# Optimization experiments

Hardware: AMD Instinct MI355X
Metric: run time of the kernel (lower is better)

The kernel has to match this reference:

```python
import jax, jax.numpy as jnp
import numpy as np

N_NODES = 100000
D = 128


def setup_inputs() -> dict:
    key = jax.random.key(0)
    ks = jax.random.split(key, 6)
    x = jax.random.normal(ks[0], (N_NODES, 300), dtype=jnp.float32)
    n_id = jnp.arange(N_NODES, dtype=jnp.int64)
    edge_index = jax.random.randint(ks[1], (2, 1600000), 0, N_NODES, dtype=jnp.int64)
    history = jax.random.randint(ks[2], (4096, 50), 0, N_NODES, dtype=jnp.int64)
    candidates = jax.random.randint(ks[3], (4096, 20), 0, N_NODES, dtype=jnp.int64)
    W_enc = jax.random.normal(ks[4], (300, D), dtype=jnp.float32) * 0.05
    W_gnn = jax.random.normal(ks[5], (D, D), dtype=jnp.float32) * 0.05
    return {"x": x, "n_id": n_id, "edge_index": edge_index,
            "history": history, "candidates": candidates,
            "W_enc": W_enc, "W_gnn": W_gnn}


def reference(x, n_id, edge_index, history, candidates, W_enc, W_gnn):
    N = x.shape[0]
    # news encoder: linear projection of raw node features -> [N, D]
    news_emb = x @ W_enc
    # gnn: mean aggregation over incoming edges, then linear
    src, dst = edge_index[0], edge_index[1]
    agg = jax.ops.segment_sum(news_emb[src], dst, num_segments=N)      # [N, D]
    deg = jax.ops.segment_sum(jnp.ones((src.shape[0], 1), news_emb.dtype), dst,
                              num_segments=N)                          # [N, 1]
    struct_emb = (agg / jnp.maximum(deg, 1.0)) @ W_gnn
    xx = news_emb + struct_emb                                          # [N, D]
    # scatter into dense lookup table (n_id == arange -> max_id == N, static)
    news_lookup = jnp.zeros((N, xx.shape[1]), xx.dtype).at[n_id].set(xx)
    # gather histories / candidates
    history_embs = news_lookup[history]                                 # [B, H, D]
    cand_embs = news_lookup[candidates]                                 # [B, C, D]
    mask = (history != 0).astype(xx.dtype)                              # [B, H]
    sum_embs = jnp.einsum('bhd,bh->bd', history_embs, mask)
    num_read = jnp.clip(mask.sum(axis=1, keepdims=True), 1e-9, None)
    user_vec = sum_embs / num_read                                      # [B, D]
    scores = jnp.einsum('bcd,bd->bc', cand_embs, user_vec)              # [B, C]
    return scores
```

## Files before the change

kernel.cpp:

```cpp
#include <hip/hip_runtime.h>

#define NN 100000
#define DD 128
#define KE 300
#define NE 1600000
#define NB 4096
#define HL 50
#define CL 20

#define NBUCK 1563
#define SLOT  1280
#define PBLK  250
#define EPB   6400
#define EPT   25
#define EBLK  1563

#define WTE_N 40960
#define WTG_N 16384

typedef unsigned short ushort_t;
using bf16x8 = __attribute__((ext_vector_type(8))) short;
using f32x4  = __attribute__((ext_vector_type(4))) float;

union U4B { uint4 u; bf16x8 b; unsigned a[4]; };

__device__ __forceinline__ ushort_t f2bf(float f) {
    unsigned u = __float_as_uint(f);
    unsigned r = u + 0x7FFF + ((u >> 16) & 1);
    return (ushort_t)(r >> 16);
}
__device__ __forceinline__ float bf2f(unsigned s) {
    return __uint_as_float(s << 16);
}
__device__ __forceinline__ bf16x8 pack8(float4 a, float4 b) {
    U4B r;
    r.a[0] = (unsigned)f2bf(a.x) | ((unsigned)f2bf(a.y) << 16);
    r.a[1] = (unsigned)f2bf(a.z) | ((unsigned)f2bf(a.w) << 16);
    r.a[2] = (unsigned)f2bf(b.x) | ((unsigned)f2bf(b.y) << 16);
    r.a[3] = (unsigned)f2bf(b.z) | ((unsigned)f2bf(b.w) << 16);
    return r.b;
}

__global__ __launch_bounds__(256) void prep_w(const float* __restrict__ We,
                                              const float* __restrict__ Wg,
                                              ushort_t* __restrict__ wte,
                                              ushort_t* __restrict__ wtg) {
    int i = blockIdx.x * 256 + threadIdx.x;
    if (i < WTE_N) {
        int j = i & 7, lane = (i >> 3) & 63, cf = (i >> 9) & 7, ch = i >> 12;
        int k = ch * 32 + (lane >> 4) * 8 + j;
        int n = cf * 16 + (lane & 15);
        wte[i] = f2bf((k < KE) ? We[k * DD + n] : 0.f);
    } else if (i < WTE_N + WTG_N) {
        int t = i - WTE_N;
        int j = t & 7, lane = (t >> 3) & 63, cf = (t >> 9) & 7, ks = t >> 12;
        int k = ks * 32 + (lane >> 4) * 8 + j;
        int n = cf * 16 + (lane & 15);
        wtg[t] = f2bf(Wg[k * DD + n]);
    }
}

__device__ __forceinline__ bf16x8 loadA8(const float* __restrict__ x,
                                         int row, int col, bool rowok) {
    float v[8];
    if (rowok && col + 8 <= KE) {
        const float4* p = (const float4*)&x[(long long)row * KE + col];
        float4 a = p[0], b = p[1];
        v[0]=a.x; v[1]=a.y; v[2]=a.z; v[3]=a.w;
        v[4]=b.x; v[5]=b.y; v[6]=b.z; v[7]=b.w;
    } else {
#pragma unroll
        for (int j = 0; j < 8; ++j) {
            int c = col + j;
            v[j] = (rowok && c < KE) ? x[(long long)row * KE + c] : 0.f;
        }
    }
    return pack8(make_float4(v[0], v[1], v[2], v[3]),
                 make_float4(v[4], v[5], v[6], v[7]));
}

__global__ __launch_bounds__(256) void k_front(const float* __restrict__ x,
                                               const ushort_t* __restrict__ wtF,
                                               const int* __restrict__ ei,
                                               unsigned* __restrict__ gcur,
                                               unsigned* __restrict__ pairs,
                                               ushort_t* __restrict__ news) {
    __shared__ unsigned sh[NBUCK], sb[NBUCK], sc[NBUCK];
    const int tid = threadIdx.x;

    if (blockIdx.x < PBLK) {
        const int eb = blockIdx.x * EPB;
        for (int i = tid; i < NBUCK; i += 256) sh[i] = 0;
        __syncthreads();

        unsigned val[EPT], bk[EPT];
#pragma unroll
        for (int l = 0; l < EPT; ++l) {
            int e = eb + l * 256 + tid;
            unsigned src = (unsigned)ei[e];
            unsigned dst = (unsigned)ei[NE + e];
            val[l] = (src << 6) | (dst & 63u);
            bk[l] = dst >> 6;
            atomicAdd(&sh[bk[l]], 1u);
        }
        __syncthreads();

        for (int i = tid; i < NBUCK; i += 256) {
            unsigned h = sh[i];
            sb[i] = (unsigned)i * SLOT + (h ? atomicAdd(&gcur[i], h) : 0u);
            sc[i] = 0;
        }
        __syncthreads();

#pragma unroll
        for (int l = 0; l < EPT; ++l) {
            unsigned b = bk[l];
            unsigned pos = sb[b] + atomicAdd(&sc[b], 1u);
            if (pos < (b + 1u) * SLOT) pairs[pos] = val[l];
        }
        return;
    }

    const int lane = tid & 63;
    const int hl = lane & 15, kg = lane >> 4;
    const int row0 = (blockIdx.x - PBLK) * 64 + (tid >> 6) * 16;
    const int r0 = row0 + hl;
    const bool ok0 = r0 < NN;

    f32x4 acc[8];
#pragma unroll
    for (int j = 0; j < 8; ++j) acc[j] = (f32x4)0.f;

#pragma unroll
    for (int p = 0; p < 5; ++p) {
        bf16x8 a0 = loadA8(x, r0, p * 64 + kg * 8, ok0);
        bf16x8 a1 = loadA8(x, r0, p * 64 + 32 + kg * 8, ok0);
#pragma unroll
        for (int ks = 0; ks < 2; ++ks) {
            bf16x8 af = ks ? a1 : a0;
            const ushort_t* bp = &wtF[((p * 2 + ks) * 8) * 512 + lane * 8];
#pragma unroll
            for (int cf = 0; cf < 8; ++cf) {
                bf16x8 bfr = *(const bf16x8*)&bp[cf * 512];
                acc[cf] = __builtin_amdgcn_mfma_f32_16x16x32_bf16(af, bfr, acc[cf], 0, 0, 0);
            }
        }
    }
#pragma unroll
    for (int cf = 0; cf < 8; ++cf)
#pragma unroll
        for (int j = 0; j < 4; ++j) {
            int grow = row0 + kg * 4 + j;
            int gcol = cf * 16 + hl;
            if (grow < NN)
                news[(long long)grow * DD + gcol] = f2bf(acc[cf][j]);
        }
}

__global__ __launch_bounds__(256) void k_baggnn(const unsigned* __restrict__ gcur,
                                                const unsigned* __restrict__ pairs,
                                                const ushort_t* __restrict__ news,
                                                const ushort_t* __restrict__ wtF,
                                                float* __restrict__ xx) {
    __shared__ unsigned srcs[SLOT];
    __shared__ unsigned hist[64], base[64], cur[64];
    __shared__ ushort_t aggs[64 * DD];
    const int tid = threadIdx.x;
    const int b = blockIdx.x;
    int cnt = (int)gcur[b];
    if (cnt > SLOT) cnt = SLOT;

    if (tid < 64) hist[tid] = 0;
    __syncthreads();
    for (int i = tid; i < cnt; i += 256)
        atomicAdd(&hist[pairs[b * SLOT + i] & 63u], 1u);
    __syncthreads();

    if (tid < 64) {
        unsigned h = hist[tid], v = h;
#pragma unroll
        for (int off = 1; off < 64; off <<= 1) {
            unsigned n = __shfl_up(v, off);
            if (tid >= off) v += n;
        }
        base[tid] = v - h;
        cur[tid]  = v - h;
    }
    __syncthreads();

    for (int i = tid; i < cnt; i += 256) {
        unsigned v = pairs[b * SLOT + i];
        srcs[atomicAdd(&cur[v & 63u], 1u)] = v >> 6;
    }
    __syncthreads();

    const int w = tid >> 6, lane = tid & 63;
    const int e = lane >> 4, l = lane & 15;
    for (int d = w; d < 64; d += 4) {
        int gd = b * 64 + d;
        if (gd >= NN) break;
        int s0 = (int)base[d], c = (int)hist[d];
        float acc[8];
#pragma unroll
        for (int j = 0; j < 8; ++j) acc[j] = 0.f;

        uint4 v = make_uint4(0u, 0u, 0u, 0u);
        if (e < c)
            v = *(const uint4*)&news[(long long)srcs[s0 + e] * DD + l * 8];
        for (int i = 4; i < c; i += 4) {
            uint4 vn = make_uint4(0u, 0u, 0u, 0u);
            int ii = i + e;
            if (ii < c)
                vn = *(const uint4*)&news[(long long)srcs[s0 + ii] * DD + l * 8];
            acc[0] += bf2f(v.x & 0xFFFFu); acc[1] += bf2f(v.x >> 16);
            acc[2] += bf2f(v.y & 0xFFFFu); acc[3] += bf2f(v.y >> 16);
            acc[4] += bf2f(v.z & 0xFFFFu); acc[5] += bf2f(v.z >> 16);
            acc[6] += bf2f(v.w & 0xFFFFu); acc[7] += bf2f(v.w >> 16);
            v = vn;
        }
        acc[0] += bf2f(v.x & 0xFFFFu); acc[1] += bf2f(v.x >> 16);
        acc[2] += bf2f(v.y & 0xFFFFu); acc[3] += bf2f(v.y >> 16);
        acc[4] += bf2f(v.z & 0xFFFFu); acc[5] += bf2f(v.z >> 16);
        acc[6] += bf2f(v.w & 0xFFFFu); acc[7] += bf2f(v.w >> 16);

#pragma unroll
        for (int j = 0; j < 8; ++j) {
            acc[j] += __shfl_xor(acc[j], 16);
            acc[j] += __shfl_xor(acc[j], 32);
        }
        if (e == 0) {
            uint4 o;
            o.x = (unsigned)f2bf(acc[0]) | ((unsigned)f2bf(acc[1]) << 16);
            o.y = (unsigned)f2bf(acc[2]) | ((unsigned)f2bf(acc[3]) << 16);
            o.z = (unsigned)f2bf(acc[4]) | ((unsigned)f2bf(acc[5]) << 16);
            o.w = (unsigned)f2bf(acc[6]) | ((unsigned)f2bf(acc[7]) << 16);
            *(uint4*)&aggs[d * DD + (l ^ (d & 15)) * 8] = o;
        }
    }
    __syncthreads();

    const int hl = lane & 15, kg = lane >> 4;
    U4B a[4];
#pragma unroll
    for (int ks = 0; ks < 4; ++ks)
        a[ks].u = *(const uint4*)&aggs[(w * 16 + hl) * DD + ((ks * 4 + kg) ^ hl) * 8];

    f32x4 acc[8];
#pragma unroll
    for (int j = 0; j < 8; ++j) acc[j] = (f32x4)0.f;

#pragma unroll
    for (int ks = 0; ks < 4; ++ks) {
        const ushort_t* bp = &wtF[(ks * 8) * 512 + lane * 8];
#pragma unroll
        for (int cf = 0; cf < 8; ++cf) {
            bf16x8 bfr = *(const bf16x8*)&bp[cf * 512];
            acc[cf] = __builtin_amdgcn_mfma_f32_16x16x32_bf16(a[ks].b, bfr, acc[cf], 0, 0, 0);
        }
    }

#pragma unroll
    for (int j = 0; j < 4; ++j) {
        int lr = w * 16 + kg * 4 + j;
        int grow = b * 64 + lr;
        if (grow < NN) {
            float s = 1.f / fmaxf((float)hist[lr], 1.f);
#pragma unroll
            for (int cf = 0; cf < 8; ++cf) {
                int gcol = cf * 16 + hl;
                float nv = bf2f((unsigned)news[(long long)grow * DD + gcol]);
                xx[(long long)grow * DD + gcol] = nv + acc[cf][j] * s;
            }
        }
    }
}

__global__ __launch_bounds__(128) void k_user(const int* __restrict__ hist,
                                              const int* __restrict__ cand,
                                              const float* __restrict__ xx,
                                              float* __restrict__ out) {
    __shared__ float uvs[128];
    const int b = blockIdx.x, t = threadIdx.x;

    float s = 0.f, cnt = 0.f;
    for (int h = 0; h < HL; ++h) {
        int id = hist[b * HL + h];
        if (id != 0) { s += xx[(long long)id * DD + t]; cnt += 1.f; }
    }
    uvs[t] = s / fmaxf(cnt, 1e-9f);
    __syncthreads();

    const int w = t >> 6, lane = t & 63;
    float2 uvp = *(const float2*)&uvs[lane * 2];
    for (int c = w; c < CL; c += 2) {
        int id = cand[b * CL + c];
        float2 xv = *(const float2*)&xx[(long long)id * DD + lane * 2];
        float p = uvp.x * xv.x + uvp.y * xv.y;
#pragma unroll
        for (int off = 32; off >= 1; off >>= 1) p += __shfl_xor(p, off);
        if (lane == 0) out[b * CL + c] = p;
    }
}

extern "C" void kernel_launch(void* const* d_in, const int* in_sizes, int n_in,
                              void* d_out, int out_size, void* d_ws, size_t ws_size,
                              hipStream_t stream) {
    const float* x    = (const float*)d_in[0];
    const int*   ei   = (const int*)d_in[2];
    const int*   hist = (const int*)d_in[3];
    const int*   cand = (const int*)d_in[4];
    const float* Wenc = (const float*)d_in[5];
    const float* Wgnn = (const float*)d_in[6];
    float* out = (float*)d_out;

    float*    xx      = (float*)d_ws;
    ushort_t* news_bf = (ushort_t*)(xx + (size_t)NN * DD);
    ushort_t* wt_enc  = news_bf + (size_t)NN * DD;
    ushort_t* wt_gnn  = wt_enc + WTE_N;
    unsigned* gcur    = (unsigned*)(wt_gnn + WTG_N);
    unsigned* pairs   = gcur + NBUCK;

    hipMemsetAsync(gcur, 0, NBUCK * sizeof(unsigned), stream);

    prep_w<<<(WTE_N + WTG_N + 255) / 256, 256, 0, stream>>>(Wenc, Wgnn, wt_enc, wt_gnn);
    k_front<<<PBLK + EBLK, 256, 0, stream>>>(x, wt_enc, ei, gcur, pairs, news_bf);
    k_baggnn<<<NBUCK, 256, 0, stream>>>(gcur, pairs, news_bf, wt_gnn, xx);
    k_user<<<NB, 128, 0, stream>>>(hist, cand, xx, out);
}
```

Before: 179.4 us.

## Split edge bucketing from encoder, make encoder persistent with register-resident weights

Edge bucketing moves out of the encoder kernel and into the weight-prep kernel. The encoder becomes a persistent kernel of 256 blocks that keeps all of W_enc in registers and loops over row tiles, loading each row slice as a batch of float4s before the MFMAs. The aggregation/GNN kernel goes to 512 threads, splitting the output columns across two groups of waves. The aim is to stop re-reading weights from global memory and to raise occupancy in the aggregation kernel. The cost is much higher register pressure, since the 80 weight fragments are held per lane.

```diff
diff --git a/kernel.cpp b/kernel.cpp
--- a/kernel.cpp
+++ b/kernel.cpp
@@ -17,6 +17,7 @@
 
 #define WTE_N 40960
 #define WTG_N 16384
+#define PREPB ((WTE_N + WTG_N + 255) / 256)
 
 typedef unsigned short ushort_t;
 using bf16x8 = __attribute__((ext_vector_type(8))) short;
@@ -41,11 +42,62 @@
     return r.b;
 }
 
-__global__ __launch_bounds__(256) void prep_w(const float* __restrict__ We,
+__device__ __forceinline__ bf16x8 loadA8m(const float* __restrict__ x,
+                                          int row, int col, bool rowok) {
+    float v[8];
+#pragma unroll
+    for (int j = 0; j < 8; ++j) {
+        int c = col + j;
+        v[j] = (rowok && c < KE) ? x[(long long)row * KE + c] : 0.f;
+    }
+    return pack8(make_float4(v[0], v[1], v[2], v[3]),
+                 make_float4(v[4], v[5], v[6], v[7]));
+}
+
+__global__ __launch_bounds__(256) void k_prep(const int* __restrict__ ei,
+                                              unsigned* __restrict__ gcur,
+                                              unsigned* __restrict__ pairs,
+                                              const float* __restrict__ We,
                                               const float* __restrict__ Wg,
                                               ushort_t* __restrict__ wte,
                                               ushort_t* __restrict__ wtg) {
-    int i = blockIdx.x * 256 + threadIdx.x;
+    __shared__ unsigned sh[NBUCK], sb[NBUCK], sc[NBUCK];
+    const int tid = threadIdx.x;
+
+    if (blockIdx.x < PBLK) {
+        const int eb = blockIdx.x * EPB;
+        for (int i = tid; i < NBUCK; i += 256) sh[i] = 0;
+        __syncthreads();
+
+        unsigned val[EPT], bk[EPT];
+#pragma unroll
+        for (int l = 0; l < EPT; ++l) {
+            int e = eb + l * 256 + tid;
+            unsigned src = (unsigned)ei[e];
+            unsigned dst = (unsigned)ei[NE + e];
+            val[l] = (src << 6) | (dst & 63u);
+            bk[l] = dst >> 6;
+            atomicAdd(&sh[bk[l]], 1u);
+        }
+        __syncthreads();
+
+        for (int i = tid; i < NBUCK; i += 256) {
+            unsigned h = sh[i];
+            sb[i] = (unsigned)i * SLOT + (h ? atomicAdd(&gcur[i], h) : 0u);
+            sc[i] = 0;
+        }
+        __syncthreads();
+
+#pragma unroll
+        for (int l = 0; l < EPT; ++l) {
+            unsigned b = bk[l];
+            unsigned pos = sb[b] + atomicAdd(&sc[b], 1u);
+            if (pos < (b + 1u) * SLOT) pairs[pos] = val[l];
+        }
+        return;
+    }
+
+    int i = (blockIdx.x - PBLK) * 256 + tid;
     if (i < WTE_N) {
         int j = i & 7, lane = (i >> 3) & 63, cf = (i >> 9) & 7, ch = i >> 12;
         int k = ch * 32 + (lane >> 4) * 8 + j;
@@ -60,104 +112,69 @@
     }
 }
 
-__device__ __forceinline__ bf16x8 loadA8(const float* __restrict__ x,
-                                         int row, int col, bool rowok) {
-    float v[8];
-    if (rowok && col + 8 <= KE) {
-        const float4* p = (const float4*)&x[(long long)row * KE + col];
-        float4 a = p[0], b = p[1];
-        v[0]=a.x; v[1]=a.y; v[2]=a.z; v[3]=a.w;
-        v[4]=b.x; v[5]=b.y; v[6]=b.z; v[7]=b.w;
-    } else {
-#pragma unroll
-        for (int j = 0; j < 8; ++j) {
-            int c = col + j;
-            v[j] = (rowok && c < KE) ? x[(long long)row * KE + c] : 0.f;
-        }
-    }
-    return pack8(make_float4(v[0], v[1], v[2], v[3]),
-                 make_float4(v[4], v[5], v[6], v[7]));
-}
-
-__global__ __launch_bounds__(256) void k_front(const float* __restrict__ x,
-                                               const ushort_t* __restrict__ wtF,
-                                               const int* __restrict__ ei,
-                                               unsigned* __restrict__ gcur,
-                                               unsigned* __restrict__ pairs,
-                                               ushort_t* __restrict__ news) {
-    __shared__ unsigned sh[NBUCK], sb[NBUCK], sc[NBUCK];
+__global__ __launch_bounds__(256, 1) void enc_mfma(const float* __restrict__ x,
+                                                   const ushort_t* __restrict__ wtF,
+                                                   ushort_t* __restrict__ news) {
     const int tid = threadIdx.x;
-
-    if (blockIdx.x < PBLK) {
-        const int eb = blockIdx.x * EPB;
-        for (int i = tid; i < NBUCK; i += 256) sh[i] = 0;
-        __syncthreads();
-
-        unsigned val[EPT], bk[EPT];
-#pragma unroll
-        for (int l = 0; l < EPT; ++l) {
-            int e = eb + l * 256 + tid;
-            unsigned src = (unsigned)ei[e];
-            unsigned dst = (unsigned)ei[NE + e];
-            val[l] = (src << 6) | (dst & 63u);
-            bk[l] = dst >> 6;
-            atomicAdd(&sh[bk[l]], 1u);
-        }
-        __syncthreads();
-
-        for (int i = tid; i < NBUCK; i += 256) {
-            unsigned h = sh[i];
-            sb[i] = (unsigned)i * SLOT + (h ? atomicAdd(&gcur[i], h) : 0u);
-            sc[i] = 0;
-        }
-        __syncthreads();
-
-#pragma unroll
-        for (int l = 0; l < EPT; ++l) {
-            unsigned b = bk[l];
-            unsigned pos = sb[b] + atomicAdd(&sc[b], 1u);
-            if (pos < (b + 1u) * SLOT) pairs[pos] = val[l];
-        }
-        return;
-    }
-
-    const int lane = tid & 63;
+    const int w = tid >> 6, lane = tid & 63;
     const int hl = lane & 15, kg = lane >> 4;
-    const int row0 = (blockIdx.x - PBLK) * 64 + (tid >> 6) * 16;
-    const int r0 = row0 + hl;
-    const bool ok0 = r0 < NN;
-
-    f32x4 acc[8];
-#pragma unroll
-    for (int j = 0; j < 8; ++j) acc[j] = (f32x4)0.f;
-
-#pragma unroll
-    for (int p = 0; p < 5; ++p) {
-        bf16x8 a0 = loadA8(x, r0, p * 64 + kg * 8, ok0);
-        bf16x8 a1 = loadA8(x, r0, p * 64 + 32 + kg * 8, ok0);
-#pragma unroll
-        for (int ks = 0; ks < 2; ++ks) {
-            bf16x8 af = ks ? a1 : a0;
-            const ushort_t* bp = &wtF[((p * 2 + ks) * 8) * 512 + lane * 8];
-#pragma unroll
-            for (int cf = 0; cf < 8; ++cf) {
-                bf16x8 bfr = *(const bf16x8*)&bp[cf * 512];
-                acc[cf] = __builtin_amdgcn_mfma_f32_16x16x32_bf16(af, bfr, acc[cf], 0, 0, 0);
+
+    bf16x8 B[10][8];
+#pragma unroll
+    for (int c = 0; c < 10; ++c)
+#pragma unroll
+        for (int cf = 0; cf < 8; ++cf)
+            B[c][cf] = *(const bf16x8*)&wtF[(c * 8 + cf) * 512 + lane * 8];
+
+    for (int tile = blockIdx.x; tile < EBLK; tile += gridDim.x) {
+        const int row0 = tile * 64 + w * 16;
+        const int r0 = row0 + hl;
+        const bool ok0 = r0 < NN;
+        const float* xr = &x[(long long)r0 * KE + kg * 8];
+        const float4 fz = make_float4(0.f, 0.f, 0.f, 0.f);
+
+        float4 ra[9][2];
+        if (ok0) {
+#pragma unroll
+            for (int c = 0; c < 9; ++c) {
+                const float4* p = (const float4*)(xr + c * 32);
+                ra[c][0] = p[0];
+                ra[c][1] = p[1];
             }
-        }
-    }
-#pragma unroll
-    for (int cf = 0; cf < 8; ++cf)
-#pragma unroll
-        for (int j = 0; j < 4; ++j) {
-            int grow = row0 + kg * 4 + j;
-            int gcol = cf * 16 + hl;
-            if (grow < NN)
-                news[(long long)grow * DD + gcol] = f2bf(acc[cf][j]);
-        }
-}
-
-__global__ __launch_bounds__(256) void k_baggnn(const unsigned* __restrict__ gcur,
+        } else {
+#pragma unroll
+            for (int c = 0; c < 9; ++c) { ra[c][0] = fz; ra[c][1] = fz; }
+        }
+        bf16x8 a9 = loadA8m(x, r0, 288 + kg * 8, ok0);
+
+        f32x4 acc[8];
+#pragma unroll
+        for (int j = 0; j < 8; ++j) acc[j] = (f32x4)0.f;
+
+#pragma unroll
+        for (int c = 0; c < 9; ++c) {
+            bf16x8 a = pack8(ra[c][0], ra[c][1]);
+#pragma unroll
+            for (int cf = 0; cf < 8; ++cf)
+                acc[cf] = __builtin_amdgcn_mfma_f32_16x16x32_bf16(a, B[c][cf], acc[cf], 0, 0, 0);
+        }
+#pragma unroll
+        for (int cf = 0; cf < 8; ++cf)
+            acc[cf] = __builtin_amdgcn_mfma_f32_16x16x32_bf16(a9, B[9][cf], acc[cf], 0, 0, 0);
+
+#pragma unroll
+        for (int cf = 0; cf < 8; ++cf)
+#pragma unroll
+            for (int j = 0; j < 4; ++j) {
+                int grow = row0 + kg * 4 + j;
+                int gcol = cf * 16 + hl;
+                if (grow < NN)
+                    news[(long long)grow * DD + gcol] = f2bf(acc[cf][j]);
+            }
+    }
+}
+
+__global__ __launch_bounds__(512) void k_baggnn(const unsigned* __restrict__ gcur,
                                                 const unsigned* __restrict__ pairs,
                                                 const ushort_t* __restrict__ news,
                                                 const ushort_t* __restrict__ wtF,
@@ -172,7 +189,7 @@
 
     if (tid < 64) hist[tid] = 0;
     __syncthreads();
-    for (int i = tid; i < cnt; i += 256)
+    for (int i = tid; i < cnt; i += 512)
         atomicAdd(&hist[pairs[b * SLOT + i] & 63u], 1u);
     __syncthreads();
 
@@ -188,7 +205,7 @@
     }
     __syncthreads();
 
-    for (int i = tid; i < cnt; i += 256) {
+    for (int i = tid; i < cnt; i += 512) {
         unsigned v = pairs[b * SLOT + i];
         srcs[atomicAdd(&cur[v & 63u], 1u)] = v >> 6;
     }
@@ -196,7 +213,7 @@
 
     const int w = tid >> 6, lane = tid & 63;
     const int e = lane >> 4, l = lane & 15;
-    for (int d = w; d < 64; d += 4) {
+    for (int d = w; d < 64; d += 8) {
         int gd = b * 64 + d;
         if (gd >= NN) break;
         int s0 = (int)base[d], c = (int)hist[d];
@@ -240,20 +257,22 @@
     __syncthreads();
 
     const int hl = lane & 15, kg = lane >> 4;
+    const int rw = (w & 3) * 16;
+    const int cfb = (w >> 2) * 4;
     U4B a[4];
 #pragma unroll
     for (int ks = 0; ks < 4; ++ks)
-        a[ks].u = *(const uint4*)&aggs[(w * 16 + hl) * DD + ((ks * 4 + kg) ^ hl) * 8];
-
-    f32x4 acc[8];
-#pragma unroll
-    for (int j = 0; j < 8; ++j) acc[j] = (f32x4)0.f;
+        a[ks].u = *(const uint4*)&aggs[(rw + hl) * DD + ((ks * 4 + kg) ^ hl) * 8];
+
+    f32x4 acc[4];
+#pragma unroll
+    for (int j = 0; j < 4; ++j) acc[j] = (f32x4)0.f;
 
 #pragma unroll
     for (int ks = 0; ks < 4; ++ks) {
-        const ushort_t* bp = &wtF[(ks * 8) * 512 + lane * 8];
-#pragma unroll
-        for (int cf = 0; cf < 8; ++cf) {
+        const ushort_t* bp = &wtF[(ks * 8 + cfb) * 512 + lane * 8];
+#pragma unroll
+        for (int cf = 0; cf < 4; ++cf) {
             bf16x8 bfr = *(const bf16x8*)&bp[cf * 512];
             acc[cf] = __builtin_amdgcn_mfma_f32_16x16x32_bf16(a[ks].b, bfr, acc[cf], 0, 0, 0);
         }
@@ -261,13 +280,13 @@
 
 #pragma unroll
     for (int j = 0; j < 4; ++j) {
-        int lr = w * 16 + kg * 4 + j;
+        int lr = rw + kg * 4 + j;
         int grow = b * 64 + lr;
         if (grow < NN) {
             float s = 1.f / fmaxf((float)hist[lr], 1.f);
 #pragma unroll
-            for (int cf = 0; cf < 8; ++cf) {
-                int gcol = cf * 16 + hl;
+            for (int cf = 0; cf < 4; ++cf) {
+                int gcol = (cfb + cf) * 16 + hl;
                 float nv = bf2f((unsigned)news[(long long)grow * DD + gcol]);
                 xx[(long long)grow * DD + gcol] = nv + acc[cf][j] * s;
             }
@@ -322,8 +341,8 @@
 
     hipMemsetAsync(gcur, 0, NBUCK * sizeof(unsigned), stream);
 
-    prep_w<<<(WTE_N + WTG_N + 255) / 256, 256, 0, stream>>>(Wenc, Wgnn, wt_enc, wt_gnn);
-    k_front<<<PBLK + EBLK, 256, 0, stream>>>(x, wt_enc, ei, gcur, pairs, news_bf);
-    k_baggnn<<<NBUCK, 256, 0, stream>>>(gcur, pairs, news_bf, wt_gnn, xx);
+    k_prep<<<PBLK + PREPB, 256, 0, stream>>>(ei, gcur, pairs, Wenc, Wgnn, wt_enc, wt_gnn);
+    enc_mfma<<<256, 256, 0, stream>>>(x, wt_enc, news_bf);
+    k_baggnn<<<NBUCK, 512, 0, stream>>>(gcur, pairs, news_bf, wt_gnn, xx);
     k_user<<<NB, 128, 0, stream>>>(hist, cand, xx, out);
 }
```

Result: faster. 169.4 us (-5.5%).
